# Kernel tuning notes

Hardware: AMD Instinct MI355X
Metric: run time of the kernel (lower is better)

Reference implementation:

```python
import jax, jax.numpy as jnp
import numpy as np

NUM_NODES = 20000
NUM_EDGES = 65536
WIDTH = 64
EDGE_FEAT = 6
HIDDEN = 128


def setup_inputs() -> dict:
    key = jax.random.key(0)
    ks = jax.random.split(key, 6)
    x = jax.random.normal(ks[0], (NUM_NODES, WIDTH), dtype=jnp.float32)
    edge_attr = jax.random.normal(ks[1], (NUM_EDGES, EDGE_FEAT), dtype=jnp.float32)
    # weight-generating MLP params (the `nn` callable), fan-in scaled
    W1 = jax.random.normal(ks[2], (EDGE_FEAT, HIDDEN), dtype=jnp.float32) / np.sqrt(EDGE_FEAT)
    b1 = jnp.zeros((HIDDEN,), dtype=jnp.float32)
    W2 = jax.random.normal(ks[3], (HIDDEN, WIDTH * WIDTH), dtype=jnp.float32) / np.sqrt(HIDDEN)
    b2 = jnp.zeros((WIDTH * WIDTH,), dtype=jnp.float32)
    senders = jax.random.randint(ks[4], (NUM_EDGES,), 0, NUM_NODES)
    receivers = jax.random.randint(ks[5], (NUM_EDGES,), 0, NUM_NODES)
    return {"x": x, "edge_attr": edge_attr, "W1": W1, "b1": b1,
            "W2": W2, "b2": b2, "senders": senders, "receivers": receivers}


def reference(x, edge_attr, W1, b1, W2, b2, senders, receivers):
    n_segs, width = x.shape
    # nn(edge_attr): (E, width*width) edge-conditioned weights
    h = jax.nn.relu(edge_attr @ W1 + b1)
    weight = (h @ W2 + b2).reshape(-1, width, width)  # (E, w, w)
    # gather sender features, per-edge (1,w) @ (w,w) matmul -> (E, w)
    msgs = jnp.einsum('ew,ewv->ev', x[senders], weight)
    # scatter-sum messages into receiver nodes (aggr == 'sum')
    return jax.ops.segment_sum(msgs, receivers, num_segments=n_segs)
```

## Files before the change

kernel.cpp:

```cpp
#include <hip/hip_runtime.h>
#include <stdint.h>

typedef _Float16 f16;
typedef f16 f16x8 __attribute__((ext_vector_type(8)));
typedef float f32x4 __attribute__((ext_vector_type(4)));

#define NUM_NODES 20000
#define NUM_EDGES 65536
#define WIDTH 64
#define EDGE_FEAT 6
#define HIDDEN 128
#define BM 128
#define NCHUNK 129
#define XPAD 72
#define HPAD 130

#define XH_HALFS (NUM_NODES * WIDTH)
#define XCONV_BLKS 625
#define W2G_HALFS (NCHUNK * 4096)
#define OUT_FLOATS (NUM_NODES * WIDTH)
#define ZBLKS 313

__device__ __forceinline__ void gload_lds16(const f16* g, f16* l) {
  __builtin_amdgcn_global_load_lds(
      (const __attribute__((address_space(1))) unsigned int*)g,
      (__attribute__((address_space(3))) unsigned int*)l, 16, 0, 0);
}

__global__ __launch_bounds__(256) void prep_kernel(
    const float* __restrict__ x, const float* __restrict__ W2,
    const float* __restrict__ b2, f16* __restrict__ ws_h,
    float* __restrict__ out)
{
  f16* x_h = ws_h;
  f16* W2g = ws_h + XH_HALFS;
  const int blk = blockIdx.x, tid = threadIdx.x;

  if (blk < NCHUNK) {
    __shared__ float row[4096];
    const int ki = blk;
    const float* srcrow;
    if (ki < HIDDEN) {
      const float4* src = (const float4*)(W2 + (size_t)ki * 4096);
      #pragma unroll
      for (int i = 0; i < 4; ++i) {
        float4 v = src[tid + 256 * i];
        *(float4*)&row[(tid + 256 * i) * 4] = v;
      }
      __syncthreads();
      srcrow = row;
    } else {
      srcrow = b2;
    }
    const int obase = tid * 16;
    f16x8 outv0, outv1;
    #pragma unroll
    for (int u = 0; u < 8; ++u) {
      int o = obase + u;
      int n = o >> 6, pg = (o >> 3) & 7, j = o & 7;
      int k = (pg ^ (n & 7)) * 8 + j;
      outv0[u] = (f16)srcrow[k * 64 + n];
    }
    #pragma unroll
    for (int u = 0; u < 8; ++u) {
      int o = obase + 8 + u;
      int n = o >> 6, pg = (o >> 3) & 7, j = o & 7;
      int k = (pg ^ (n & 7)) * 8 + j;
      outv1[u] = (f16)srcrow[k * 64 + n];
    }
    *(f16x8*)&W2g[(size_t)ki * 4096 + obase] = outv0;
    *(f16x8*)&W2g[(size_t)ki * 4096 + obase + 8] = outv1;
  } else if (blk < NCHUNK + XCONV_BLKS) {
    int idx = (blk - NCHUNK) * 2048 + tid * 8;
    if (idx + 8 <= XH_HALFS) {
      float4 a = *(const float4*)(x + idx);
      float4 b = *(const float4*)(x + idx + 4);
      f16x8 hv;
      hv[0] = (f16)a.x; hv[1] = (f16)a.y; hv[2] = (f16)a.z; hv[3] = (f16)a.w;
      hv[4] = (f16)b.x; hv[5] = (f16)b.y; hv[6] = (f16)b.z; hv[7] = (f16)b.w;
      *(f16x8*)&x_h[idx] = hv;
    }
  } else {
    int base = (blk - NCHUNK - XCONV_BLKS) * 4096 + tid * 16;
    float4 z = {0.f, 0.f, 0.f, 0.f};
    #pragma unroll
    for (int i = 0; i < 4; ++i) {
      int idx = base + i * 4;
      if (idx + 4 <= OUT_FLOATS) *(float4*)(out + idx) = z;
    }
  }
}

__global__ __launch_bounds__(256, 2) void nnconv_kernel(
    const float* __restrict__ ea, const float* __restrict__ W1,
    const float* __restrict__ b1, const int* __restrict__ senders,
    const int* __restrict__ receivers, const f16* __restrict__ ws_h,
    float* __restrict__ out)
{
  const f16* x_h = ws_h;
  const f16* W2g = ws_h + XH_HALFS;
  __shared__ __align__(16) f16 xt[BM][XPAD];
  __shared__ __align__(16) f16 hbuf[HIDDEN * HPAD];
  __shared__ __align__(16) f16 ring[3 * 4096];

  const int tid = threadIdx.x;
  const int lane = tid & 63, wid = tid >> 6;
  const int quad = lane >> 4, l15 = lane & 15;
  const int mhalf = wid >> 1, nhalf = wid & 1;
  const int e0 = blockIdx.x * BM;
  const int mbase = mhalf * 64;

  const f16* wsrc = W2g + wid * 1024 + (lane << 3);
  const int stg_off = wid * 1024;

  gload_lds16(wsrc, &ring[stg_off]);
  gload_lds16(wsrc + 512, &ring[stg_off + 512]);
  gload_lds16(wsrc + 4096, &ring[4096 + stg_off]);
  gload_lds16(wsrc + 4096 + 512, &ring[4096 + stg_off + 512]);

  float* eaf = (float*)&ring[2 * 4096];
  if (tid < 192)
    ((float4*)eaf)[tid] = ((const float4*)(ea + (size_t)e0 * EDGE_FEAT))[tid];

  {
    int r = tid >> 1, half = tid & 1;
    int s = senders[e0 + r];
    const uint4* src = (const uint4*)(x_h + (size_t)s * WIDTH + half * 32);
    uint4* dst = (uint4*)&xt[r][half * 32];
    #pragma unroll
    for (int i = 0; i < 4; ++i) dst[i] = src[i];
  }

  __syncthreads();

  {
    const int k = tid >> 1, half = tid & 1;
    float b1c = b1[k];
    float w1c[6];
    #pragma unroll
    for (int f = 0; f < 6; ++f) w1c[f] = W1[f * HIDDEN + k];
    f16* hrow = &hbuf[k * HPAD + half * 64];
    const float* er = eaf + half * 64 * EDGE_FEAT;
    #pragma unroll 2
    for (int g8 = 0; g8 < 8; ++g8) {
      f16x8 hv;
      #pragma unroll
      for (int j = 0; j < 8; ++j) {
        const float* p = er + (g8 * 8 + j) * EDGE_FEAT;
        float s = b1c;
        #pragma unroll
        for (int f = 0; f < 6; ++f) s = fmaf(p[f], w1c[f], s);
        hv[j] = (f16)fmaxf(s, 0.f);
      }
      *(f16x8*)&hrow[g8 * 8] = hv;
    }
  }

  f16x8 xf[4][2];
  #pragma unroll
  for (int t = 0; t < 4; ++t)
    #pragma unroll
    for (int kc = 0; kc < 2; ++kc)
      xf[t][kc] = *(const f16x8*)&xt[mbase + t * 16 + l15][kc * 32 + quad * 8];

  int boff[2][2];
  #pragma unroll
  for (int kc = 0; kc < 2; ++kc)
    #pragma unroll
    for (int nt = 0; nt < 2; ++nt) {
      int n = nhalf * 32 + nt * 16 + l15;
      int g = kc * 4 + quad;
      boff[kc][nt] = n * 64 + (g ^ (n & 7)) * 8;
    }

  const f16* hb = &hbuf[mbase + l15];

  f32x4 acc[4][2];
  #pragma unroll
  for (int t = 0; t < 4; ++t)
    #pragma unroll
    for (int nt = 0; nt < 2; ++nt)
      acc[t][nt] = (f32x4){0.f, 0.f, 0.f, 0.f};

  __syncthreads();

#define STEP(K, SLOT, STG, SDST, VM)                                          \
  {                                                                           \
    asm volatile("s_waitcnt vmcnt(%0) lgkmcnt(0)\n\ts_barrier"                \
                 :: "i"(VM) : "memory");                                      \
    __builtin_amdgcn_sched_barrier(0);                                        \
    if (STG) {                                                                \
      const f16* s_ = wsrc + (size_t)((K) + 2) * 4096;                        \
      f16* d_ = &ring[(SDST) * 4096 + stg_off];                               \
      gload_lds16(s_, d_);                                                    \
      gload_lds16(s_ + 512, d_ + 512);                                        \
    }                                                                         \
    __builtin_amdgcn_sched_barrier(0);                                        \
    f16 hv_[4];                                                               \
    _Pragma("unroll") for (int t = 0; t < 4; ++t)                             \
      hv_[t] = hb[(K) * HPAD + t * 16];                                       \
    const f16* gb_ = &ring[(SLOT) * 4096];                                    \
    f16x8 bf_[2][2];                                                          \
    _Pragma("unroll") for (int kc = 0; kc < 2; ++kc)                          \
      _Pragma("unroll") for (int nt = 0; nt < 2; ++nt)                        \
        bf_[kc][nt] = *(const f16x8*)&gb_[boff[kc][nt]];                      \
    f16x8 sa0_[4], sa1_[4];                                                   \
    _Pragma("unroll") for (int t = 0; t < 4; ++t) {                           \
      sa0_[t] = xf[t][0] * hv_[t];                                            \
      sa1_[t] = xf[t][1] * hv_[t];                                            \
    }                                                                         \
    __builtin_amdgcn_s_setprio(1);                                            \
    _Pragma("unroll") for (int t = 0; t < 4; ++t)                             \
      _Pragma("unroll") for (int nt = 0; nt < 2; ++nt)                        \
        acc[t][nt] = __builtin_amdgcn_mfma_f32_16x16x32_f16(                  \
            sa0_[t], bf_[0][nt], acc[t][nt], 0, 0, 0);                        \
    _Pragma("unroll") for (int t = 0; t < 4; ++t)                             \
      _Pragma("unroll") for (int nt = 0; nt < 2; ++nt)                        \
        acc[t][nt] = __builtin_amdgcn_mfma_f32_16x16x32_f16(                  \
            sa1_[t], bf_[1][nt], acc[t][nt], 0, 0, 0);                        \
    __builtin_amdgcn_s_setprio(0);                                            \
  }

  #pragma unroll 1
  for (int kb = 0; kb < 126; kb += 6) {
    STEP(kb + 0, 0, 1, 2, 2);
    STEP(kb + 1, 1, 1, 0, 2);
    STEP(kb + 2, 2, 1, 1, 2);
    STEP(kb + 3, 0, 1, 2, 2);
    STEP(kb + 4, 1, 1, 0, 2);
    STEP(kb + 5, 2, 1, 1, 2);
  }
  STEP(126, 0, 1, 2, 2);
  STEP(127, 1, 0, 0, 2);

  asm volatile("s_waitcnt vmcnt(0) lgkmcnt(0)\n\ts_barrier" ::: "memory");
  __builtin_amdgcn_sched_barrier(0);
  {
    const f16* gb_ = &ring[2 * 4096];
    f16x8 bf_[2][2];
    #pragma unroll
    for (int kc = 0; kc < 2; ++kc)
      #pragma unroll
      for (int nt = 0; nt < 2; ++nt)
        bf_[kc][nt] = *(const f16x8*)&gb_[boff[kc][nt]];
    __builtin_amdgcn_s_setprio(1);
    #pragma unroll
    for (int t = 0; t < 4; ++t)
      #pragma unroll
      for (int nt = 0; nt < 2; ++nt) {
        acc[t][nt] = __builtin_amdgcn_mfma_f32_16x16x32_f16(
            xf[t][0], bf_[0][nt], acc[t][nt], 0, 0, 0);
        acc[t][nt] = __builtin_amdgcn_mfma_f32_16x16x32_f16(
            xf[t][1], bf_[1][nt], acc[t][nt], 0, 0, 0);
      }
    __builtin_amdgcn_s_setprio(0);
  }
#undef STEP

  #pragma unroll
  for (int t = 0; t < 4; ++t) {
    int ebase = e0 + mbase + t * 16 + quad * 4;
    int rc[4];
    #pragma unroll
    for (int r = 0; r < 4; ++r) rc[r] = receivers[ebase + r];
    #pragma unroll
    for (int nt = 0; nt < 2; ++nt) {
      int v = (nhalf * 2 + nt) * 16 + l15;
      #pragma unroll
      for (int r = 0; r < 4; ++r)
        atomicAdd(out + (size_t)rc[r] * WIDTH + v, acc[t][nt][r]);
    }
  }
}

extern "C" void kernel_launch(void* const* d_in, const int* in_sizes, int n_in,
                              void* d_out, int out_size, void* d_ws, size_t ws_size,
                              hipStream_t stream) {
  const float* x  = (const float*)d_in[0];
  const float* ea = (const float*)d_in[1];
  const float* W1 = (const float*)d_in[2];
  const float* b1 = (const float*)d_in[3];
  const float* W2 = (const float*)d_in[4];
  const float* b2 = (const float*)d_in[5];
  const int* snd  = (const int*)d_in[6];
  const int* rcv  = (const int*)d_in[7];
  float* out = (float*)d_out;
  f16* wsh = (f16*)d_ws;

  const int prep_grid = NCHUNK + XCONV_BLKS + ZBLKS;
  prep_kernel<<<prep_grid, 256, 0, stream>>>(x, W2, b2, wsh, out);
  nnconv_kernel<<<NUM_EDGES / BM, 256, 0, stream>>>(ea, W1, b1, snd, rcv, wsh, out);
}
```

Baseline: 145.7 us.

## Stage W2 in two-chunk groups with double buffering and load sender rows directly

The main loop now stages two 4096-element W2 chunks per step into a two-slot LDS ring. This halves the number of barrier and wait points, at the cost of a shorter prefetch distance with vmcnt(0) waits. The prep kernel pads the converted weight buffer with zero chunks so the grouping covers the bias chunk evenly. Sender feature fragments are read straight from global memory into registers, dropping the LDS staging tile. The h buffer padding is also removed, which shrinks LDS but may add bank conflicts on writes.

```diff
diff --git a/kernel.cpp b/kernel.cpp
--- a/kernel.cpp
+++ b/kernel.cpp
@@ -11,13 +11,10 @@
 #define EDGE_FEAT 6
 #define HIDDEN 128
 #define BM 128
-#define NCHUNK 129
-#define XPAD 72
-#define HPAD 130
+#define PADCH 132
 
 #define XH_HALFS (NUM_NODES * WIDTH)
 #define XCONV_BLKS 625
-#define W2G_HALFS (NCHUNK * 4096)
 #define OUT_FLOATS (NUM_NODES * WIDTH)
 #define ZBLKS 313
 
@@ -36,9 +33,17 @@
   f16* W2g = ws_h + XH_HALFS;
   const int blk = blockIdx.x, tid = threadIdx.x;
 
-  if (blk < NCHUNK) {
+  if (blk < PADCH) {
+    const int ki = blk;
+    if (ki > HIDDEN) {
+      f16x8 z;
+      #pragma unroll
+      for (int u = 0; u < 8; ++u) z[u] = (f16)0.f;
+      *(f16x8*)&W2g[(size_t)ki * 4096 + tid * 16] = z;
+      *(f16x8*)&W2g[(size_t)ki * 4096 + tid * 16 + 8] = z;
+      return;
+    }
     __shared__ float row[4096];
-    const int ki = blk;
     const float* srcrow;
     if (ki < HIDDEN) {
       const float4* src = (const float4*)(W2 + (size_t)ki * 4096);
@@ -70,8 +75,8 @@
     }
     *(f16x8*)&W2g[(size_t)ki * 4096 + obase] = outv0;
     *(f16x8*)&W2g[(size_t)ki * 4096 + obase + 8] = outv1;
-  } else if (blk < NCHUNK + XCONV_BLKS) {
-    int idx = (blk - NCHUNK) * 2048 + tid * 8;
+  } else if (blk < PADCH + XCONV_BLKS) {
+    int idx = (blk - PADCH) * 2048 + tid * 8;
     if (idx + 8 <= XH_HALFS) {
       float4 a = *(const float4*)(x + idx);
       float4 b = *(const float4*)(x + idx + 4);
@@ -81,7 +86,7 @@
       *(f16x8*)&x_h[idx] = hv;
     }
   } else {
-    int base = (blk - NCHUNK - XCONV_BLKS) * 4096 + tid * 16;
+    int base = (blk - PADCH - XCONV_BLKS) * 4096 + tid * 16;
     float4 z = {0.f, 0.f, 0.f, 0.f};
     #pragma unroll
     for (int i = 0; i < 4; ++i) {
@@ -99,9 +104,8 @@
 {
   const f16* x_h = ws_h;
   const f16* W2g = ws_h + XH_HALFS;
-  __shared__ __align__(16) f16 xt[BM][XPAD];
-  __shared__ __align__(16) f16 hbuf[HIDDEN * HPAD];
-  __shared__ __align__(16) f16 ring[3 * 4096];
+  __shared__ __align__(16) f16 hbuf[HIDDEN * 128];
+  __shared__ __align__(16) f16 ring[2 * 8192];
 
   const int tid = threadIdx.x;
   const int lane = tid & 63, wid = tid >> 6;
@@ -110,25 +114,27 @@
   const int e0 = blockIdx.x * BM;
   const int mbase = mhalf * 64;
 
-  const f16* wsrc = W2g + wid * 1024 + (lane << 3);
-  const int stg_off = wid * 1024;
-
-  gload_lds16(wsrc, &ring[stg_off]);
-  gload_lds16(wsrc + 512, &ring[stg_off + 512]);
-  gload_lds16(wsrc + 4096, &ring[4096 + stg_off]);
-  gload_lds16(wsrc + 4096 + 512, &ring[4096 + stg_off + 512]);
-
-  float* eaf = (float*)&ring[2 * 4096];
+  const f16* wsl = W2g + wid * 2048 + (lane << 3);
+  #pragma unroll
+  for (int i = 0; i < 4; ++i)
+    gload_lds16(wsl + i * 512, &ring[wid * 2048 + i * 512]);
+
+  float* eaf = (float*)&ring[8192];
   if (tid < 192)
     ((float4*)eaf)[tid] = ((const float4*)(ea + (size_t)e0 * EDGE_FEAT))[tid];
 
+  f16x8 xf[4][2];
   {
-    int r = tid >> 1, half = tid & 1;
-    int s = senders[e0 + r];
-    const uint4* src = (const uint4*)(x_h + (size_t)s * WIDTH + half * 32);
-    uint4* dst = (uint4*)&xt[r][half * 32];
-    #pragma unroll
-    for (int i = 0; i < 4; ++i) dst[i] = src[i];
+    int srows[4];
+    #pragma unroll
+    for (int t = 0; t < 4; ++t)
+      srows[t] = senders[e0 + mbase + t * 16 + l15];
+    #pragma unroll
+    for (int t = 0; t < 4; ++t)
+      #pragma unroll
+      for (int kc = 0; kc < 2; ++kc)
+        xf[t][kc] = *(const f16x8*)(x_h + (size_t)srows[t] * WIDTH +
+                                    kc * 32 + quad * 8);
   }
 
   __syncthreads();
@@ -139,7 +145,7 @@
     float w1c[6];
     #pragma unroll
     for (int f = 0; f < 6; ++f) w1c[f] = W1[f * HIDDEN + k];
-    f16* hrow = &hbuf[k * HPAD + half * 64];
+    f16* hrow = &hbuf[k * 128 + half * 64];
     const float* er = eaf + half * 64 * EDGE_FEAT;
     #pragma unroll 2
     for (int g8 = 0; g8 < 8; ++g8) {
@@ -156,13 +162,6 @@
     }
   }
 
-  f16x8 xf[4][2];
-  #pragma unroll
-  for (int t = 0; t < 4; ++t)
-    #pragma unroll
-    for (int kc = 0; kc < 2; ++kc)
-      xf[t][kc] = *(const f16x8*)&xt[mbase + t * 16 + l15][kc * 32 + quad * 8];
-
   int boff[2][2];
   #pragma unroll
   for (int kc = 0; kc < 2; ++kc)
@@ -184,26 +183,15 @@
 
   __syncthreads();
 
-#define STEP(K, SLOT, STG, SDST, VM)                                          \
+#define CHUNK(CB, HK)                                                         \
   {                                                                           \
-    asm volatile("s_waitcnt vmcnt(%0) lgkmcnt(0)\n\ts_barrier"                \
-                 :: "i"(VM) : "memory");                                      \
-    __builtin_amdgcn_sched_barrier(0);                                        \
-    if (STG) {                                                                \
-      const f16* s_ = wsrc + (size_t)((K) + 2) * 4096;                        \
-      f16* d_ = &ring[(SDST) * 4096 + stg_off];                               \
-      gload_lds16(s_, d_);                                                    \
-      gload_lds16(s_ + 512, d_ + 512);                                        \
-    }                                                                         \
-    __builtin_amdgcn_sched_barrier(0);                                        \
-    f16 hv_[4];                                                               \
-    _Pragma("unroll") for (int t = 0; t < 4; ++t)                             \
-      hv_[t] = hb[(K) * HPAD + t * 16];                                       \
-    const f16* gb_ = &ring[(SLOT) * 4096];                                    \
     f16x8 bf_[2][2];                                                          \
     _Pragma("unroll") for (int kc = 0; kc < 2; ++kc)                          \
       _Pragma("unroll") for (int nt = 0; nt < 2; ++nt)                        \
-        bf_[kc][nt] = *(const f16x8*)&gb_[boff[kc][nt]];                      \
+        bf_[kc][nt] = *(const f16x8*)&(CB)[boff[kc][nt]];                     \
+    f16 hv_[4];                                                               \
+    _Pragma("unroll") for (int t = 0; t < 4; ++t)                             \
+      hv_[t] = hb[(HK) * 128 + t * 16];                                       \
     f16x8 sa0_[4], sa1_[4];                                                   \
     _Pragma("unroll") for (int t = 0; t < 4; ++t) {                           \
       sa0_[t] = xf[t][0] * hv_[t];                                            \
@@ -221,28 +209,38 @@
     __builtin_amdgcn_s_setprio(0);                                            \
   }
 
+#define GSTEP(G, SL, SD)                                                      \
+  {                                                                           \
+    asm volatile("s_waitcnt vmcnt(0) lgkmcnt(0)\n\ts_barrier" ::: "memory");  \
+    __builtin_amdgcn_sched_barrier(0);                                        \
+    {                                                                         \
+      const f16* s_ = wsl + (size_t)((G) + 1) * 8192;                         \
+      f16* d_ = &ring[(SD) * 8192 + wid * 2048];                              \
+      _Pragma("unroll") for (int i_ = 0; i_ < 4; ++i_)                        \
+        gload_lds16(s_ + i_ * 512, d_ + i_ * 512);                            \
+    }                                                                         \
+    __builtin_amdgcn_sched_barrier(0);                                        \
+    const f16* gb_ = &ring[(SL) * 8192];                                      \
+    CHUNK(gb_, 2 * (G));                                                      \
+    CHUNK(gb_ + 4096, 2 * (G) + 1);                                           \
+  }
+
   #pragma unroll 1
-  for (int kb = 0; kb < 126; kb += 6) {
-    STEP(kb + 0, 0, 1, 2, 2);
-    STEP(kb + 1, 1, 1, 0, 2);
-    STEP(kb + 2, 2, 1, 1, 2);
-    STEP(kb + 3, 0, 1, 2, 2);
-    STEP(kb + 4, 1, 1, 0, 2);
-    STEP(kb + 5, 2, 1, 1, 2);
-  }
-  STEP(126, 0, 1, 2, 2);
-  STEP(127, 1, 0, 0, 2);
+  for (int g = 0; g < 64; g += 2) {
+    GSTEP(g,     0, 1);
+    GSTEP(g + 1, 1, 0);
+  }
+#undef GSTEP
 
   asm volatile("s_waitcnt vmcnt(0) lgkmcnt(0)\n\ts_barrier" ::: "memory");
   __builtin_amdgcn_sched_barrier(0);
   {
-    const f16* gb_ = &ring[2 * 4096];
     f16x8 bf_[2][2];
     #pragma unroll
     for (int kc = 0; kc < 2; ++kc)
       #pragma unroll
       for (int nt = 0; nt < 2; ++nt)
-        bf_[kc][nt] = *(const f16x8*)&gb_[boff[kc][nt]];
+        bf_[kc][nt] = *(const f16x8*)&ring[boff[kc][nt]];
     __builtin_amdgcn_s_setprio(1);
     #pragma unroll
     for (int t = 0; t < 4; ++t)
@@ -255,7 +253,7 @@
       }
     __builtin_amdgcn_s_setprio(0);
   }
-#undef STEP
+#undef CHUNK
 
   #pragma unroll
   for (int t = 0; t < 4; ++t) {
@@ -287,7 +285,7 @@
   float* out = (float*)d_out;
   f16* wsh = (f16*)d_ws;
 
-  const int prep_grid = NCHUNK + XCONV_BLKS + ZBLKS;
+  const int prep_grid = PADCH + XCONV_BLKS + ZBLKS;
   prep_kernel<<<prep_grid, 256, 0, stream>>>(x, W2, b2, wsh, out);
   nnconv_kernel<<<NUM_EDGES / BM, 256, 0, stream>>>(ea, W1, b1, snd, rcv, wsh, out);
 }
```

After: 144.8 us (median of 2 runs). No clear change (-0.7%).
